# Kernel optimization log

Measured on AMD Instinct MI355X. Metric: run time of the kernel, lower is better.

## Reference

```python
import jax, jax.numpy as jnp
import numpy as np

B, S, D, NH = 4, 1024, 512, 8
HD = D // NH
KN, KL, NC, V = 16384, 8, 4, 6400
EPS = 1e-5
TEMP = 1.0


def _rms(x, w):
    return x * jax.lax.rsqrt(jnp.mean(x * x, axis=-1, keepdims=True) + EPS) * w


def _rope(x, cos, sin):
    # x: [b,s,h,hd]; cos/sin: [s,hd//2] (rotary pairs, minimind complex style)
    xr, xi = x[..., ::2], x[..., 1::2]
    c = cos[None, :, None, :]
    s = sin[None, :, None, :]
    yr = xr * c - xi * s
    yi = xr * s + xi * c
    return jnp.stack([yr, yi], axis=-1).reshape(x.shape)


def setup_inputs() -> dict:
    key = jax.random.key(0)
    ks = jax.random.split(key, 12)
    sc = lambda n: 1.0 / np.sqrt(n)
    inv = 1.0 / (10000.0 ** (np.arange(0, HD, 2) / HD))
    freqs = np.outer(np.arange(S), inv).astype(np.float32)  # [S, HD//2]
    return {
        "x": jax.random.normal(ks[0], (B, S, D), jnp.float32),
        "pos_cos": jnp.asarray(np.cos(freqs)),
        "pos_sin": jnp.asarray(np.sin(freqs)),
        "memory_bank": jax.random.randint(ks[1], (KN, KL), 0, V),
        "tok_emb": jax.random.normal(ks[2], (V, D), jnp.float32) * 0.02,
        "wq": jax.random.normal(ks[3], (D, D), jnp.float32) * sc(D),
        "wk": jax.random.normal(ks[4], (D, D), jnp.float32) * sc(D),
        "wv": jax.random.normal(ks[5], (D, D), jnp.float32) * sc(D),
        "wo": jax.random.normal(ks[6], (D, D), jnp.float32) * sc(D),
        "attn_norm_w": jnp.ones((D,), jnp.float32),
        "mem_norm_w": jnp.ones((D,), jnp.float32),
        "w_gate": jax.random.normal(ks[7], (D, KN), jnp.float32) * sc(D),
        "wg_fuse": jax.random.normal(ks[8], (2 * D, D), jnp.float32) * sc(2 * D),
        "bg_fuse": jnp.zeros((D,), jnp.float32),
        "wm_fuse": jax.random.normal(ks[9], (2 * D, D), jnp.float32) * sc(2 * D),
        "bm_fuse": jnp.zeros((D,), jnp.float32),
        "gumbel_u": jax.random.uniform(ks[10], (B, S, NC), jnp.float32),
    }


def reference(x, pos_cos, pos_sin, memory_bank, tok_emb, wq, wk, wv, wo,
              attn_norm_w, mem_norm_w, w_gate, wg_fuse, bg_fuse, wm_fuse,
              bm_fuse, gumbel_u):
    # --- self attention on attention_norm(x) ---
    hn = _rms(x, attn_norm_w)
    q = _rope((hn @ wq).reshape(B, S, NH, HD), pos_cos, pos_sin)
    k = _rope((hn @ wk).reshape(B, S, NH, HD), pos_cos, pos_sin)
    v = (hn @ wv).reshape(B, S, NH, HD)
    att = jnp.einsum('bqhd,bkhd->bhqk', q, k) * (1.0 / np.sqrt(HD))
    causal = jnp.tril(jnp.ones((S, S), bool))
    att = jnp.where(causal, att, jnp.float32(-1e9))
    p = jax.nn.softmax(att, axis=-1)
    h_attn = jnp.einsum('bhqk,bkhd->bqhd', p, v).reshape(B, S, D) @ wo
    h = x + h_attn

    # --- memory gate: route each token to NC candidate memories ---
    hm = _rms(h_attn, mem_norm_w)                      # memory_norm(h_attn)
    logits = hm @ w_gate                               # [B,S,KN]
    _scores, cand_idx = jax.lax.top_k(logits, NC)      # [B,S,NC]

    # gather memory token ids, embed, mean-pool over knowledge_length
    tok_ids = memory_bank[cand_idx]                    # [B,S,NC,KL]
    cand_mem = tok_emb[tok_ids].mean(axis=3)           # [B,S,NC,D]

    # cosine similarity (torch eps=1e-8 clamp on norms)
    hn2 = jnp.maximum(jnp.linalg.norm(hm, axis=-1), 1e-8)          # [B,S]
    cn2 = jnp.maximum(jnp.linalg.norm(cand_mem, axis=-1), 1e-8)    # [B,S,NC]
    sim = jnp.einsum('bsd,bsnd->bsn', hm, cand_mem) / (hn2[:, :, None] * cn2)

    # gumbel-softmax hard selection with straight-through estimator
    g = -jnp.log(-jnp.log(gumbel_u + 1e-20) + 1e-20)
    soft = jax.nn.softmax((sim + g) / TEMP, axis=-1)
    hard = jax.nn.one_hot(jnp.argmax(soft, axis=-1), NC, dtype=soft.dtype)
    sel_w = hard - jax.lax.stop_gradient(soft) + soft

    similarity_loss = -(sim * sel_w).sum(-1).mean()

    # diversity loss: mean off-diagonal cosine similarity among candidates
    nm = cand_mem / jnp.maximum(jnp.linalg.norm(cand_mem, axis=-1, keepdims=True), 1e-12)
    smat = jnp.einsum('bsnd,bsmd->bsnm', nm, nm)
    eye = jnp.eye(NC, dtype=bool)
    diversity_loss = jnp.where(eye, 0.0, smat).sum() / (B * S * NC * (NC - 1))

    # weighted combine + gated fusion
    sel_mem = jnp.einsum('bsn,bsnd->bsd', sel_w, cand_mem)
    cat = jnp.concatenate([hm, sel_mem], axis=-1)      # [B,S,2D]
    gate = jax.nn.sigmoid(cat @ wg_fuse + bg_fuse)
    memory_output = gate * (cat @ wm_fuse + bm_fuse)
    out = h + memory_output
    return out, similarity_loss, diversity_loss
```

## Files before the change

kernel.cpp:

```cpp
#include <hip/hip_runtime.h>
#include <hip/hip_bf16.h>
#include <math.h>

#define Bn 4
#define Sn 1024
#define Dn 512
#define NHn 8
#define HDn 64
#define KNn 16384
#define KLn 8
#define NCn 4
#define Mn (Bn*Sn)

typedef __attribute__((ext_vector_type(8))) short short8;
typedef __attribute__((ext_vector_type(4))) float f32x4;
typedef unsigned long long u64;

#define MFMA16(a,b,c) __builtin_amdgcn_mfma_f32_16x16x32_bf16(a,b,c,0,0,0)


__device__ __forceinline__ float wred_sum(float v){
  #pragma unroll
  for (int m=1;m<64;m<<=1) v += __shfl_xor(v, m, 64);
  return v;
}

__device__ __forceinline__ ushort f2bf(float f){
  __hip_bfloat16 h = __float2bfloat16(f);
  return __builtin_bit_cast(ushort, h);
}
__device__ __forceinline__ float bf2f(ushort u){
  return __builtin_bit_cast(float, ((unsigned)u)<<16);
}

__device__ __forceinline__ unsigned int fkey(float v){
  unsigned int b = __builtin_bit_cast(unsigned int, v);
  return (b & 0x80000000u) ? ~b : (b | 0x80000000u);
}
__device__ __forceinline__ u64 mkkey(float v, int col){
  return ((u64)fkey(v) << 32) | (u64)(0xFFFFu - (unsigned)col);
}

__device__ __forceinline__ void cex64(u64& a, u64& b){
  u64 mx = a > b ? a : b;
  u64 mn = a > b ? b : a;
  a = mx; b = mn;
}
__device__ __forceinline__ void ins4_64(u64 k, u64&k0,u64&k1,u64&k2,u64&k3){
  if (k > k3){
    k3 = k;
    cex64(k2,k3); cex64(k1,k2); cex64(k0,k1);
  }
}
__device__ __forceinline__ void merge4_64(u64&a0,u64&a1,u64&a2,u64&a3,
                                          u64 b0,u64 b1,u64 b2,u64 b3){
  cex64(a0,b3); cex64(a1,b2); cex64(a2,b1); cex64(a3,b0);
  cex64(a0,a2); cex64(a1,a3);
  cex64(a0,a1); cex64(a2,a3);
}


__global__ __launch_bounds__(256) void rmsnorm_kernel(const float* __restrict__ x,
                                                      const float* __restrict__ w,
                                                      ushort* __restrict__ y){
  int row = blockIdx.x, tid = threadIdx.x;
  const float2* xr = (const float2*)(x + (size_t)row*Dn);
  float2 v = xr[tid];
  float ss = v.x*v.x + v.y*v.y;
  ss = wred_sum(ss);
  __shared__ float red[4];
  int wid = tid>>6, lane = tid&63;
  if (lane==0) red[wid]=ss;
  __syncthreads();
  float tot = red[0]+red[1]+red[2]+red[3];
  float sc = rsqrtf(tot*(1.0f/Dn) + 1e-5f);
  float2 wv = ((const float2*)w)[tid];
  ushort2 u; u.x = f2bf(v.x*sc*wv.x); u.y = f2bf(v.y*sc*wv.y);
  *(ushort2*)&y[(size_t)row*Dn + tid*2] = u;
}


__global__ __launch_bounds__(256) void convT_kernel(const float* __restrict__ src,
                                                    ushort* __restrict__ dst,
                                                    int ldsrc, int lddst){
  __shared__ float T[64][68];
  int tid=threadIdx.x;
  int n0 = blockIdx.x*64, k0 = blockIdx.y*64;
  #pragma unroll
  for (int h=0;h<4;h++){
    int idx = tid + h*256;
    int r = idx>>4, c = (idx&15)*4;
    float4 v = *(const float4*)&src[(size_t)(k0+r)*ldsrc + n0+c];
    *(float4*)&T[r][c] = v;
  }
  __syncthreads();
  #pragma unroll
  for (int h=0;h<4;h++){
    int idx = tid + h*256;
    int n = idx>>4, kc = (idx&15)*4;
    ushort4 u;
    u.x = f2bf(T[kc+0][n]);
    u.y = f2bf(T[kc+1][n]);
    u.z = f2bf(T[kc+2][n]);
    u.w = f2bf(T[kc+3][n]);
    *(ushort4*)&dst[(size_t)(n0+n)*lddst + k0+kc] = u;
  }
}


template<int MODE>
__global__ __launch_bounds__(256) void gemm_bf16(const ushort* __restrict__ A, int lda,
                                                 const ushort* __restrict__ BT, int K,
                                                 void* __restrict__ Cv, int ldc,
                                                 const float* __restrict__ pc,
                                                 const float* __restrict__ ps){
  __shared__ __align__(16) ushort As[64*72];
  __shared__ __align__(16) ushort Bs[64*72];
  int tid=threadIdx.x;
  int w = tid>>6, l = tid&63;
  int wr = w>>1, wc = w&1;
  int g = l>>4, li = l&15;
  int m0 = blockIdx.y*64, n0 = blockIdx.x*64;
  f32x4 acc[2][2] = {};
  for (int kt=0; kt<K; kt+=64){
    #pragma unroll
    for (int t=0;t<2;t++){
      int ch = tid + t*256;
      int r = ch>>3, c = (ch&7)*8;
      *(uint4*)&As[r*72+c] = *(const uint4*)&A [(size_t)(m0+r)*lda + kt + c];
      *(uint4*)&Bs[r*72+c] = *(const uint4*)&BT[(size_t)(n0+r)*K   + kt + c];
    }
    __syncthreads();
    #pragma unroll
    for (int kk=0;kk<2;kk++){
      short8 a0 = *(const short8*)&As[(wr*32 +      li)*72 + kk*32 + g*8];
      short8 a1 = *(const short8*)&As[(wr*32 + 16 + li)*72 + kk*32 + g*8];
      short8 b0 = *(const short8*)&Bs[(wc*32 +      li)*72 + kk*32 + g*8];
      short8 b1 = *(const short8*)&Bs[(wc*32 + 16 + li)*72 + kk*32 + g*8];
      acc[0][0] = MFMA16(a0, b0, acc[0][0]);
      acc[0][1] = MFMA16(a0, b1, acc[0][1]);
      acc[1][0] = MFMA16(a1, b0, acc[1][0]);
      acc[1][1] = MFMA16(a1, b1, acc[1][1]);
    }
    __syncthreads();
  }
  #pragma unroll
  for (int mi=0;mi<2;mi++){
    #pragma unroll
    for (int ni=0;ni<2;ni++){
      #pragma unroll
      for (int reg=0;reg<4;reg++){
        int mm = m0 + wr*32 + mi*16 + g*4 + reg;
        int n  = n0 + wc*32 + ni*16 + li;
        float val = acc[mi][ni][reg];
        if (MODE==0){
          ((float*)Cv)[(size_t)mm*ldc + n] = val;
        } else if (MODE==3){
          ((ushort*)Cv)[(size_t)mm*ldc + n] = f2bf(val);
        } else {
          int b = mm>>10, s2 = mm&1023, h = n>>6, d = n&63;
          size_t o = ((size_t)(b*NHn + h)*Sn + s2)*HDn + d;
          if (MODE==2){
            ((ushort*)Cv)[o] = f2bf(val);
          } else {
            float other = __shfl_xor(val, 1, 64);
            float cc = pc[s2*32 + (d>>1)], snv = ps[s2*32 + (d>>1)];
            float rv = ((li&1)==0) ? val*cc - other*snv : other*snv + val*cc;
            ((ushort*)Cv)[o] = f2bf(rv);
          }
        }
      }
    }
  }
}


__global__ __launch_bounds__(256) void attn_mfma(const ushort* __restrict__ q,
                                                 const ushort* __restrict__ k,
                                                 const ushort* __restrict__ v,
                                                 ushort* __restrict__ o){
  __shared__ __align__(16) ushort Ks[64*72];
  __shared__ __align__(16) ushort VTs[64*64];
  __shared__ __align__(16) ushort Ps[4][16*72];
  int tid = threadIdx.x;
  int w = tid>>6, l = tid&63;
  int g = l>>4, li = l&15;
  int qt = blockIdx.x, bh = blockIdx.y;
  const ushort* Qg = q + ((size_t)bh*Sn + qt*64 + w*16)*HDn;
  const ushort* Kg = k + (size_t)bh*Sn*HDn;
  const ushort* Vg = v + (size_t)bh*Sn*HDn;
  short8 aq0 = *(const short8*)&Qg[(size_t)li*HDn + g*8];
  short8 aq1 = *(const short8*)&Qg[(size_t)li*HDn + 32 + g*8];
  f32x4 oacc[4] = {};
  float mreg[4] = {-1e30f,-1e30f,-1e30f,-1e30f};
  float lreg[4] = {0.f,0.f,0.f,0.f};
  for (int kt=0; kt<=qt; kt++){
    #pragma unroll
    for (int t=0;t<2;t++){
      int ch = tid + t*256;
      int r = ch>>3, c = (ch&7)*8;
      short8 kv8 = *(const short8*)&Kg[(size_t)(kt*64+r)*HDn + c];
      short8 vv8 = *(const short8*)&Vg[(size_t)(kt*64+r)*HDn + c];
      *(short8*)&Ks[r*72 + c] = kv8;
      #pragma unroll
      for (int j=0;j<8;j++){
        int d = c+j;
        int byteoff = d*128 + ((((r>>3) ^ (d>>3)) & 7)<<4) + (r&7)*2;
        *(ushort*)((char*)VTs + byteoff) = (ushort)vv8[j];
      }
    }
    __syncthreads();
    f32x4 s[4] = {};
    #pragma unroll
    for (int n=0;n<4;n++){
      short8 b0 = *(const short8*)&Ks[(n*16+li)*72 + g*8];
      short8 b1 = *(const short8*)&Ks[(n*16+li)*72 + 32 + g*8];
      s[n] = MFMA16(aq0, b0, s[n]);
      s[n] = MFMA16(aq1, b1, s[n]);
    }
    if (kt == qt){
      #pragma unroll
      for (int n=0;n<4;n++){
        int kvg = n*16 + li;
        #pragma unroll
        for (int reg=0;reg<4;reg++){
          int qg = w*16 + g*4 + reg;
          s[n][reg] = (kvg <= qg) ? s[n][reg]*0.125f : -1e9f;
        }
      }
    } else {
      #pragma unroll
      for (int n=0;n<4;n++)
        #pragma unroll
        for (int reg=0;reg<4;reg++) s[n][reg] *= 0.125f;
    }
    #pragma unroll
    for (int reg=0;reg<4;reg++){
      float mt = fmaxf(fmaxf(s[0][reg],s[1][reg]), fmaxf(s[2][reg],s[3][reg]));
      mt = fmaxf(mt, __shfl_xor(mt,1,64));
      mt = fmaxf(mt, __shfl_xor(mt,2,64));
      mt = fmaxf(mt, __shfl_xor(mt,4,64));
      mt = fmaxf(mt, __shfl_xor(mt,8,64));
      float mn = fmaxf(mreg[reg], mt);
      float sc = __expf(mreg[reg]-mn);
      mreg[reg] = mn;
      float p0 = __expf(s[0][reg]-mn), p1 = __expf(s[1][reg]-mn);
      float p2 = __expf(s[2][reg]-mn), p3 = __expf(s[3][reg]-mn);
      s[0][reg]=p0; s[1][reg]=p1; s[2][reg]=p2; s[3][reg]=p3;
      float sm = p0+p1+p2+p3;
      sm += __shfl_xor(sm,1,64);
      sm += __shfl_xor(sm,2,64);
      sm += __shfl_xor(sm,4,64);
      sm += __shfl_xor(sm,8,64);
      lreg[reg] = lreg[reg]*sc + sm;
      #pragma unroll
      for (int n=0;n<4;n++) oacc[n][reg] *= sc;
    }
    #pragma unroll
    for (int n=0;n<4;n++)
      #pragma unroll
      for (int reg=0;reg<4;reg++)
        Ps[w][(g*4+reg)*72 + n*16 + li] = f2bf(s[n][reg]);
    #pragma unroll
    for (int kk=0;kk<2;kk++){
      short8 ap = *(const short8*)&Ps[w][li*72 + kk*32 + g*8];
      #pragma unroll
      for (int n=0;n<4;n++){
        int d = n*16 + li;
        int gran = ((kk*4 + g) ^ (d>>3)) & 7;
        short8 bv = *(const short8*)((char*)VTs + d*128 + (gran<<4));
        oacc[n] = MFMA16(ap, bv, oacc[n]);
      }
    }
    __syncthreads();
  }
  int b = bh>>3, h = bh&7;
  #pragma unroll
  for (int reg=0;reg<4;reg++){
    int qg = qt*64 + w*16 + g*4 + reg;
    float inv = 1.f/lreg[reg];
    #pragma unroll
    for (int n=0;n<4;n++)
      o[((size_t)(b*Sn+qg))*Dn + h*HDn + n*16 + li] = f2bf(oacc[n][reg]*inv);
  }
}


__global__ __launch_bounds__(256) void h_hm_kernel(const float* __restrict__ x,
                                                   const ushort* __restrict__ ha,
                                                   const float* __restrict__ w,
                                                   float* __restrict__ h,
                                                   float* __restrict__ hm32,
                                                   ushort* __restrict__ cat_bf){
  int row=blockIdx.x, tid=threadIdx.x;
  ushort2 a2 = *(const ushort2*)&ha[(size_t)row*Dn + tid*2];
  float ax = bf2f(a2.x), ay = bf2f(a2.y);
  float2 xv = ((const float2*)(x + (size_t)row*Dn))[tid];
  float ss = ax*ax + ay*ay;
  ss = wred_sum(ss);
  __shared__ float red[4];
  int wid=tid>>6, lane=tid&63;
  if (lane==0) red[wid]=ss;
  __syncthreads();
  float tot = red[0]+red[1]+red[2]+red[3];
  float sc = rsqrtf(tot*(1.0f/Dn) + 1e-5f);
  float2 wv = ((const float2*)w)[tid];
  float hm0 = ax*sc*wv.x, hm1 = ay*sc*wv.y;
  ((float2*)(h + (size_t)row*Dn))[tid] = make_float2(xv.x+ax, xv.y+ay);
  ((float2*)(hm32 + (size_t)row*Dn))[tid] = make_float2(hm0, hm1);
  ushort2 u; u.x = f2bf(hm0); u.y = f2bf(hm1);
  *(ushort2*)&cat_bf[(size_t)row*1024 + tid*2] = u;
}


__global__ __launch_bounds__(256) void logits_topk_mfma(const ushort* __restrict__ Abf,
                                                        const ushort* __restrict__ BT,
                                                        u64* __restrict__ keys){
  __shared__ __align__(16) char smem[2*128*40*2];
  ushort* As = (ushort*)smem;
  ushort* Bs = (ushort*)(smem + 128*40*2);
  float*  Ls = (float*)smem;
  int tid=threadIdx.x;
  int w = tid>>6, l = tid&63;
  int wr = w>>1, wc = w&1;
  int g = l>>4, li = l&15;
  int m0 = blockIdx.y*128, n0 = blockIdx.x*128;
  f32x4 acc[4][4] = {};
  for (int kt=0; kt<Dn; kt+=32){
    #pragma unroll
    for (int t=0;t<2;t++){
      int ch = tid + t*256;
      int r = ch>>2, c = (ch&3)*8;
      *(uint4*)&As[r*40+c] = *(const uint4*)&Abf[(size_t)(m0+r)*1024 + kt + c];
      *(uint4*)&Bs[r*40+c] = *(const uint4*)&BT [(size_t)(n0+r)*Dn   + kt + c];
    }
    __syncthreads();
    short8 a[4], b[4];
    #pragma unroll
    for (int i=0;i<4;i++) a[i] = *(const short8*)&As[(wr*64 + i*16 + li)*40 + g*8];
    #pragma unroll
    for (int n=0;n<4;n++) b[n] = *(const short8*)&Bs[(wc*64 + n*16 + li)*40 + g*8];
    #pragma unroll
    for (int i=0;i<4;i++)
      #pragma unroll
      for (int n=0;n<4;n++)
        acc[i][n] = MFMA16(a[i], b[n], acc[i][n]);
    __syncthreads();
  }
  for (int i=0;i<4;i++){
    #pragma unroll
    for (int n=0;n<4;n++)
      #pragma unroll
      for (int reg=0;reg<4;reg++)
        Ls[(wr*16 + g*4 + reg)*132 + wc*64 + n*16 + li] = acc[i][n][reg];
    __syncthreads();
    {
      int r = tid>>3, s = tid&7;
      u64 k0=0,k1=0,k2=0,k3=0;
      #pragma unroll
      for (int c4=0;c4<4;c4++){
        float4 vv = *(const float4*)&Ls[r*132 + s*16 + c4*4];
        int cb = n0 + s*16 + c4*4;
        ins4_64(mkkey(vv.x, cb+0), k0,k1,k2,k3);
        ins4_64(mkkey(vv.y, cb+1), k0,k1,k2,k3);
        ins4_64(mkkey(vv.z, cb+2), k0,k1,k2,k3);
        ins4_64(mkkey(vv.w, cb+3), k0,k1,k2,k3);
      }
      #pragma unroll
      for (int mask=1; mask<8; mask<<=1){
        u64 b0=__shfl_xor(k0,mask,64), b1=__shfl_xor(k1,mask,64);
        u64 b2=__shfl_xor(k2,mask,64), b3=__shfl_xor(k3,mask,64);
        merge4_64(k0,k1,k2,k3, b0,b1,b2,b3);
      }
      if (s==0){
        size_t grow = m0 + ((r>>4)*64 + i*16 + (r&15));
        size_t ob = (grow*128 + blockIdx.x)*4;
        keys[ob+0]=k0; keys[ob+1]=k1; keys[ob+2]=k2; keys[ob+3]=k3;
      }
    }
    __syncthreads();
  }
}


__global__ __launch_bounds__(256) void merge_topk_kernel(const u64* __restrict__ keys,
                                                         int* __restrict__ cand){
  int tid=threadIdx.x, wid=tid>>6, lane=tid&63;
  int row = blockIdx.x*4 + wid;
  size_t base = (size_t)row*512 + (size_t)lane*8;
  u64 k0=keys[base+0],k1=keys[base+1],k2=keys[base+2],k3=keys[base+3];
  merge4_64(k0,k1,k2,k3, keys[base+4],keys[base+5],keys[base+6],keys[base+7]);
  #pragma unroll
  for (int mask=1; mask<64; mask<<=1){
    u64 b0=__shfl_xor(k0,mask,64), b1=__shfl_xor(k1,mask,64);
    u64 b2=__shfl_xor(k2,mask,64), b3=__shfl_xor(k3,mask,64);
    merge4_64(k0,k1,k2,k3, b0,b1,b2,b3);
  }
  if (lane==0){
    cand[(size_t)row*4+0]=(int)(0xFFFFu - (unsigned)(k0 & 0xFFFFu));
    cand[(size_t)row*4+1]=(int)(0xFFFFu - (unsigned)(k1 & 0xFFFFu));
    cand[(size_t)row*4+2]=(int)(0xFFFFu - (unsigned)(k2 & 0xFFFFu));
    cand[(size_t)row*4+3]=(int)(0xFFFFu - (unsigned)(k3 & 0xFFFFu));
  }
}


__global__ __launch_bounds__(256) void select_kernel(const float* __restrict__ hm32,
                                                     const int* __restrict__ cand,
                                                     const int* __restrict__ mem_bank,
                                                     const float* __restrict__ tok_emb,
                                                     const float* __restrict__ gu,
                                                     ushort* __restrict__ cat_bf,
                                                     float* __restrict__ losses){
  __shared__ float cm[4][512];
  __shared__ int ids[32];
  __shared__ float wred[15][4];
  __shared__ int sel_s;
  int row=blockIdx.x, tid=threadIdx.x;
  if (tid<32) ids[tid] = mem_bank[(size_t)cand[(size_t)row*4 + (tid>>3)]*KLn + (tid&7)];
  __syncthreads();
  #pragma unroll
  for (int n=0;n<4;n++){
    float s0=0.f, s1=0.f;
    #pragma unroll
    for (int l=0;l<8;l++){
      const float* e = tok_emb + (size_t)ids[n*8+l]*Dn;
      s0 += e[tid]; s1 += e[tid+256];
    }
    cm[n][tid]=s0*0.125f; cm[n][tid+256]=s1*0.125f;
  }
  __syncthreads();
  float hm0 = hm32[(size_t)row*Dn + tid], hm1 = hm32[(size_t)row*Dn + 256 + tid];
  float c0[4], c1[4];
  #pragma unroll
  for (int n=0;n<4;n++){ c0[n]=cm[n][tid]; c1[n]=cm[n][tid+256]; }
  float p[15];
  p[0]=hm0*hm0+hm1*hm1;
  #pragma unroll
  for (int n=0;n<4;n++) p[1+n]=hm0*c0[n]+hm1*c1[n];
  int qi=5;
  #pragma unroll
  for (int n=0;n<4;n++)
    #pragma unroll
    for (int m=n;m<4;m++) p[qi++]=c0[n]*c0[m]+c1[n]*c1[m];
  int wid=tid>>6, lane=tid&63;
  #pragma unroll
  for (int i=0;i<15;i++) p[i]=wred_sum(p[i]);
  if (lane==0){
    #pragma unroll
    for (int i=0;i<15;i++) wred[i][wid]=p[i];
  }
  __syncthreads();
  if (tid==0){
    float tot[15];
    #pragma unroll
    for (int i=0;i<15;i++) tot[i]=wred[i][0]+wred[i][1]+wred[i][2]+wred[i][3];
    float hn2 = fmaxf(sqrtf(tot[0]), 1e-8f);
    const int diag[4]={5,9,12,14};
    float sim[4], dn[4];
    #pragma unroll
    for (int n=0;n<4;n++){
      float cn = sqrtf(tot[diag[n]]);
      sim[n] = tot[1+n]/(hn2*fmaxf(cn,1e-8f));
      dn[n]  = fmaxf(cn,1e-12f);
    }
    float best=-1e30f; int sel=0;
    #pragma unroll
    for (int n=0;n<4;n++){
      float u = gu[(size_t)row*4+n];
      float g = -logf(-logf(u + 1e-20f) + 1e-20f);
      float a = sim[n]+g;
      if (a>best){ best=a; sel=n; }
    }
    atomicAdd(&losses[0], sim[sel]);
    const int cross[6]={6,7,8,10,11,13};
    const int cn_[6]={0,0,0,1,1,2}, cm_[6]={1,2,3,2,3,3};
    float dv=0.f;
    #pragma unroll
    for (int t=0;t<6;t++) dv += 2.f*tot[cross[t]]/(dn[cn_[t]]*dn[cm_[t]]);
    atomicAdd(&losses[1], dv);
    sel_s=sel;
  }
  __syncthreads();
  int sel=sel_s;
  cat_bf[(size_t)row*1024 + 512 + tid]       = f2bf(cm[sel][tid]);
  cat_bf[(size_t)row*1024 + 512 + 256 + tid] = f2bf(cm[sel][tid+256]);
}


__global__ __launch_bounds__(256) void final_kernel(const float* __restrict__ h,
                                                    const float* __restrict__ g,
                                                    const float* __restrict__ m,
                                                    const float* __restrict__ bg,
                                                    const float* __restrict__ bm,
                                                    const float* __restrict__ losses,
                                                    float* __restrict__ out){
  int idx = blockIdx.x*256 + threadIdx.x;
  int n = idx & (Dn-1);
  float gl = g[idx] + bg[n];
  float ml = m[idx] + bm[n];
  float gate = 1.f/(1.f+__expf(-gl));
  out[idx] = h[idx] + gate*ml;
  if (idx==0){
    out[(size_t)Mn*Dn]     = -losses[0]*(1.f/(float)Mn);
    out[(size_t)Mn*Dn + 1] =  losses[1]*(1.f/(float)(Mn*NCn*(NCn-1)));
  }
}


extern "C" void kernel_launch(void* const* d_in, const int* in_sizes, int n_in,
                              void* d_out, int out_size, void* d_ws, size_t ws_size,
                              hipStream_t stream){
  const float* x           = (const float*)d_in[0];
  const float* pos_cos     = (const float*)d_in[1];
  const float* pos_sin     = (const float*)d_in[2];
  const int*   memory_bank = (const int*)  d_in[3];
  const float* tok_emb     = (const float*)d_in[4];
  const float* wq          = (const float*)d_in[5];
  const float* wk          = (const float*)d_in[6];
  const float* wv          = (const float*)d_in[7];
  const float* wo          = (const float*)d_in[8];
  const float* attn_norm_w = (const float*)d_in[9];
  const float* mem_norm_w  = (const float*)d_in[10];
  const float* w_gate      = (const float*)d_in[11];
  const float* wg_fuse     = (const float*)d_in[12];
  const float* bg_fuse     = (const float*)d_in[13];
  const float* wm_fuse     = (const float*)d_in[14];
  const float* bm_fuse     = (const float*)d_in[15];
  const float* gumbel_u    = (const float*)d_in[16];
  float* out = (float*)d_out;

  char* ws = (char*)d_ws;
  const size_t MB = 1u<<20;
  ushort* BTg       = (ushort*)(ws);
  ushort* wqT       = (ushort*)(ws + 16*MB);
  ushort* wkT       = (ushort*)(ws + 16*MB + 512*1024);
  ushort* wvT       = (ushort*)(ws + 17*MB);
  ushort* woT       = (ushort*)(ws + 17*MB + 512*1024);
  ushort* wgfT      = (ushort*)(ws + 18*MB);
  ushort* wmfT      = (ushort*)(ws + 19*MB);
  ushort* hn_bf     = (ushort*)(ws + 20*MB);
  ushort* pv_bf     = (ushort*)(ws + 20*MB);
  ushort* qb_bf     = (ushort*)(ws + 24*MB);
  ushort* kb_bf     = (ushort*)(ws + 28*MB);
  ushort* vb_bf     = (ushort*)(ws + 32*MB);
  ushort* h_attn_bf = (ushort*)(ws + 36*MB);
  float*  hbuf      = (float*)(ws + 40*MB);
  float*  hm32      = (float*)(ws + 48*MB);
  ushort* cat_bf    = (ushort*)(ws + 56*MB);
  u64*    keys      = (u64*)  (ws + 20*MB);
  float*  gbuf      = (float*)(ws + 20*MB);
  float*  mbuf      = (float*)(ws + 28*MB);
  int*    cand      = (int*)  (ws + 64*MB);
  float*  losses    = (float*)(ws + 64*MB + 65536);

  hipMemsetAsync(losses, 0, 2*sizeof(float), stream);

  convT_kernel<<<dim3(8,8),   256, 0, stream>>>(wq,      wqT,  512,  512);
  convT_kernel<<<dim3(8,8),   256, 0, stream>>>(wk,      wkT,  512,  512);
  convT_kernel<<<dim3(8,8),   256, 0, stream>>>(wv,      wvT,  512,  512);
  convT_kernel<<<dim3(8,8),   256, 0, stream>>>(wo,      woT,  512,  512);
  convT_kernel<<<dim3(8,16),  256, 0, stream>>>(wg_fuse, wgfT, 512,  1024);
  convT_kernel<<<dim3(8,16),  256, 0, stream>>>(wm_fuse, wmfT, 512,  1024);
  convT_kernel<<<dim3(256,8), 256, 0, stream>>>(w_gate,  BTg,  KNn,  512);

  rmsnorm_kernel<<<Mn, 256, 0, stream>>>(x, attn_norm_w, hn_bf);

  dim3 g64(Dn/64, Mn/64);
  gemm_bf16<1><<<g64, 256, 0, stream>>>(hn_bf, 512, wqT, 512, qb_bf, 0, pos_cos, pos_sin);
  gemm_bf16<1><<<g64, 256, 0, stream>>>(hn_bf, 512, wkT, 512, kb_bf, 0, pos_cos, pos_sin);
  gemm_bf16<2><<<g64, 256, 0, stream>>>(hn_bf, 512, wvT, 512, vb_bf, 0, nullptr, nullptr);

  attn_mfma<<<dim3(Sn/64, Bn*NHn), 256, 0, stream>>>(qb_bf, kb_bf, vb_bf, pv_bf);

  gemm_bf16<3><<<g64, 256, 0, stream>>>(pv_bf, 512, woT, 512, h_attn_bf, 512, nullptr, nullptr);

  h_hm_kernel<<<Mn, 256, 0, stream>>>(x, h_attn_bf, mem_norm_w, hbuf, hm32, cat_bf);

  logits_topk_mfma<<<dim3(KNn/128, Mn/128), 256, 0, stream>>>(cat_bf, BTg, keys);
  merge_topk_kernel<<<Mn/4, 256, 0, stream>>>(keys, cand);

  select_kernel<<<Mn, 256, 0, stream>>>(hm32, cand, memory_bank, tok_emb, gumbel_u, cat_bf, losses);

  gemm_bf16<0><<<g64, 256, 0, stream>>>(cat_bf, 1024, wgfT, 1024, gbuf, 512, nullptr, nullptr);
  gemm_bf16<0><<<g64, 256, 0, stream>>>(cat_bf, 1024, wmfT, 1024, mbuf, 512, nullptr, nullptr);

  final_kernel<<<(Mn*Dn)/256, 256, 0, stream>>>(hbuf, gbuf, mbuf, bg_fuse, bm_fuse, losses, out);
}
```

Measured before the change: 563.7 us.

## Replace in-GEMM top-k with group-max, group top-4, and exact recompute; fuse QKV and fuse GEMMs

```diff
diff --git a/kernel.cpp b/kernel.cpp
--- a/kernel.cpp
+++ b/kernel.cpp
@@ -37,8 +37,8 @@
   unsigned int b = __builtin_bit_cast(unsigned int, v);
   return (b & 0x80000000u) ? ~b : (b | 0x80000000u);
 }
-__device__ __forceinline__ u64 mkkey(float v, int col){
-  return ((u64)fkey(v) << 32) | (u64)(0xFFFFu - (unsigned)col);
+__device__ __forceinline__ u64 mkkey(float v, int idx){
+  return ((u64)fkey(v) << 32) | (u64)(0xFFFFu - (unsigned)idx);
 }
 
 __device__ __forceinline__ void cex64(u64& a, u64& b){
@@ -80,12 +80,11 @@
 }
 
 
-__global__ __launch_bounds__(256) void convT_kernel(const float* __restrict__ src,
-                                                    ushort* __restrict__ dst,
-                                                    int ldsrc, int lddst){
+__device__ __forceinline__ void convT_body(const float* __restrict__ src,
+                                           ushort* __restrict__ dst,
+                                           int ldsrc, int lddst,
+                                           int n0, int k0, int tid){
   __shared__ float T[64][68];
-  int tid=threadIdx.x;
-  int n0 = blockIdx.x*64, k0 = blockIdx.y*64;
   #pragma unroll
   for (int h=0;h<4;h++){
     int idx = tid + h*256;
@@ -105,6 +104,30 @@
     u.w = f2bf(T[kc+3][n]);
     *(ushort4*)&dst[(size_t)(n0+n)*lddst + k0+kc] = u;
   }
+}
+
+__global__ __launch_bounds__(256) void convT_kernel(const float* __restrict__ src,
+                                                    ushort* __restrict__ dst,
+                                                    int ldsrc, int lddst){
+  convT_body(src, dst, ldsrc, lddst, blockIdx.x*64, blockIdx.y*64, threadIdx.x);
+}
+
+__global__ __launch_bounds__(256) void convT4_kernel(const float* __restrict__ s0,
+                                                     const float* __restrict__ s1,
+                                                     const float* __restrict__ s2,
+                                                     const float* __restrict__ s3,
+                                                     ushort* __restrict__ dst){
+  const float* src = (blockIdx.z==0)?s0 : (blockIdx.z==1)?s1 : (blockIdx.z==2)?s2 : s3;
+  convT_body(src, dst + (size_t)blockIdx.z*(512*512), 512, 512,
+             blockIdx.x*64, blockIdx.y*64, threadIdx.x);
+}
+
+__global__ __launch_bounds__(256) void convT2_kernel(const float* __restrict__ s0,
+                                                     const float* __restrict__ s1,
+                                                     ushort* __restrict__ dst){
+  const float* src = (blockIdx.z==0)?s0 : s1;
+  convT_body(src, dst + (size_t)blockIdx.z*(512*1024), 512, 1024,
+             blockIdx.x*64, blockIdx.y*64, threadIdx.x);
 }
 
 
@@ -158,9 +181,11 @@
         } else if (MODE==3){
           ((ushort*)Cv)[(size_t)mm*ldc + n] = f2bf(val);
         } else {
-          int b = mm>>10, s2 = mm&1023, h = n>>6, d = n&63;
-          size_t o = ((size_t)(b*NHn + h)*Sn + s2)*HDn + d;
-          if (MODE==2){
+          int which = n>>9, nn = n&511;
+          int b = mm>>10, s2 = mm&1023, h = nn>>6, d = nn&63;
+          size_t o = (size_t)which*((size_t)Mn*Dn)
+                   + ((size_t)(b*NHn + h)*Sn + s2)*HDn + d;
+          if (which==2){
             ((ushort*)Cv)[o] = f2bf(val);
           } else {
             float other = __shfl_xor(val, 1, 64);
@@ -313,13 +338,11 @@
 }
 
 
-__global__ __launch_bounds__(256) void logits_topk_mfma(const ushort* __restrict__ Abf,
-                                                        const ushort* __restrict__ BT,
-                                                        u64* __restrict__ keys){
-  __shared__ __align__(16) char smem[2*128*40*2];
-  ushort* As = (ushort*)smem;
-  ushort* Bs = (ushort*)(smem + 128*40*2);
-  float*  Ls = (float*)smem;
+__global__ __launch_bounds__(256) void logits_gmax(const ushort* __restrict__ Abf,
+                                                   const ushort* __restrict__ BT,
+                                                   float* __restrict__ gmaxT){
+  __shared__ __align__(16) ushort As[128*40];
+  __shared__ __align__(16) ushort Bs[128*40];
   int tid=threadIdx.x;
   int w = tid>>6, l = tid&63;
   int wr = w>>1, wc = w&1;
@@ -344,63 +367,95 @@
     for (int i=0;i<4;i++)
       #pragma unroll
       for (int n=0;n<4;n++)
-        acc[i][n] = MFMA16(a[i], b[n], acc[i][n]);
+        acc[i][n] = MFMA16(b[n], a[i], acc[i][n]);
     __syncthreads();
   }
+  #pragma unroll
   for (int i=0;i<4;i++){
     #pragma unroll
-    for (int n=0;n<4;n++)
-      #pragma unroll
-      for (int reg=0;reg<4;reg++)
-        Ls[(wr*16 + g*4 + reg)*132 + wc*64 + n*16 + li] = acc[i][n][reg];
-    __syncthreads();
-    {
-      int r = tid>>3, s = tid&7;
-      u64 k0=0,k1=0,k2=0,k3=0;
-      #pragma unroll
-      for (int c4=0;c4<4;c4++){
-        float4 vv = *(const float4*)&Ls[r*132 + s*16 + c4*4];
-        int cb = n0 + s*16 + c4*4;
-        ins4_64(mkkey(vv.x, cb+0), k0,k1,k2,k3);
-        ins4_64(mkkey(vv.y, cb+1), k0,k1,k2,k3);
-        ins4_64(mkkey(vv.z, cb+2), k0,k1,k2,k3);
-        ins4_64(mkkey(vv.w, cb+3), k0,k1,k2,k3);
-      }
-      #pragma unroll
-      for (int mask=1; mask<8; mask<<=1){
-        u64 b0=__shfl_xor(k0,mask,64), b1=__shfl_xor(k1,mask,64);
-        u64 b2=__shfl_xor(k2,mask,64), b3=__shfl_xor(k3,mask,64);
-        merge4_64(k0,k1,k2,k3, b0,b1,b2,b3);
-      }
-      if (s==0){
-        size_t grow = m0 + ((r>>4)*64 + i*16 + (r&15));
-        size_t ob = (grow*128 + blockIdx.x)*4;
-        keys[ob+0]=k0; keys[ob+1]=k1; keys[ob+2]=k2; keys[ob+3]=k3;
-      }
-    }
-    __syncthreads();
-  }
-}
-
-
-__global__ __launch_bounds__(256) void merge_topk_kernel(const u64* __restrict__ keys,
-                                                         int* __restrict__ cand){
-  int tid=threadIdx.x, wid=tid>>6, lane=tid&63;
+    for (int n=0;n<4;n++){
+      f32x4 v = acc[i][n];
+      float m = fmaxf(fmaxf(v[0],v[1]), fmaxf(v[2],v[3]));
+      m = fmaxf(m, __shfl_xor(m,16,64));
+      m = fmaxf(m, __shfl_xor(m,32,64));
+      if (g==0)
+        gmaxT[(size_t)(blockIdx.x*8 + wc*4 + n)*Mn + (m0 + wr*64 + i*16 + li)] = m;
+    }
+  }
+}
+
+
+__global__ __launch_bounds__(256) void gmerge_kernel(const float* __restrict__ gmaxT,
+                                                     int* __restrict__ gidx){
+  __shared__ u64 part[64][4][4];
+  int tid=threadIdx.x;
+  int rl = tid&63, ch = tid>>6;
+  int row = blockIdx.x*64 + rl;
+  u64 k0=0,k1=0,k2=0,k3=0;
+  for (int s=0;s<256;s++){
+    int gid = ch*256 + s;
+    float v = gmaxT[(size_t)gid*Mn + row];
+    ins4_64(mkkey(v, gid), k0,k1,k2,k3);
+  }
+  part[rl][ch][0]=k0; part[rl][ch][1]=k1; part[rl][ch][2]=k2; part[rl][ch][3]=k3;
+  __syncthreads();
+  if (tid<64){
+    u64 a0=part[tid][0][0],a1=part[tid][0][1],a2=part[tid][0][2],a3=part[tid][0][3];
+    merge4_64(a0,a1,a2,a3, part[tid][1][0],part[tid][1][1],part[tid][1][2],part[tid][1][3]);
+    merge4_64(a0,a1,a2,a3, part[tid][2][0],part[tid][2][1],part[tid][2][2],part[tid][2][3]);
+    merge4_64(a0,a1,a2,a3, part[tid][3][0],part[tid][3][1],part[tid][3][2],part[tid][3][3]);
+    int r2 = blockIdx.x*64 + tid;
+    gidx[(size_t)r2*4+0] = (int)(0xFFFFu - (unsigned)(a0 & 0xFFFFu));
+    gidx[(size_t)r2*4+1] = (int)(0xFFFFu - (unsigned)(a1 & 0xFFFFu));
+    gidx[(size_t)r2*4+2] = (int)(0xFFFFu - (unsigned)(a2 & 0xFFFFu));
+    gidx[(size_t)r2*4+3] = (int)(0xFFFFu - (unsigned)(a3 & 0xFFFFu));
+  }
+}
+
+
+__global__ __launch_bounds__(256) void recompute_kernel(const ushort* __restrict__ cat_bf,
+                                                        const ushort* __restrict__ BT,
+                                                        const int* __restrict__ gidx,
+                                                        int* __restrict__ cand){
+  __shared__ float hmf[4][512];
+  int tid=threadIdx.x, wid=tid>>6, l=tid&63;
   int row = blockIdx.x*4 + wid;
-  size_t base = (size_t)row*512 + (size_t)lane*8;
-  u64 k0=keys[base+0],k1=keys[base+1],k2=keys[base+2],k3=keys[base+3];
-  merge4_64(k0,k1,k2,k3, keys[base+4],keys[base+5],keys[base+6],keys[base+7]);
+  {
+    uint4 raw = *(const uint4*)&cat_bf[(size_t)row*1024 + l*8];
+    const ushort* u = (const ushort*)&raw;
+    float4 f0 = make_float4(bf2f(u[0]),bf2f(u[1]),bf2f(u[2]),bf2f(u[3]));
+    float4 f1 = make_float4(bf2f(u[4]),bf2f(u[5]),bf2f(u[6]),bf2f(u[7]));
+    *(float4*)&hmf[wid][l*8]   = f0;
+    *(float4*)&hmf[wid][l*8+4] = f1;
+  }
+  __syncthreads();
+  int gid = gidx[(size_t)row*4 + (l>>4)];
+  int col = gid*16 + (l&15);
+  const ushort* bp = BT + (size_t)col*Dn;
+  float a0=0.f,a1=0.f,a2=0.f,a3=0.f;
+  #pragma unroll 8
+  for (int j=0;j<64;j++){
+    short8 bb = *(const short8*)&bp[j*8];
+    float4 h0 = *(const float4*)&hmf[wid][j*8];
+    float4 h1 = *(const float4*)&hmf[wid][j*8+4];
+    a0 += h0.x*bf2f((ushort)bb[0]) + h1.x*bf2f((ushort)bb[4]);
+    a1 += h0.y*bf2f((ushort)bb[1]) + h1.y*bf2f((ushort)bb[5]);
+    a2 += h0.z*bf2f((ushort)bb[2]) + h1.z*bf2f((ushort)bb[6]);
+    a3 += h0.w*bf2f((ushort)bb[3]) + h1.w*bf2f((ushort)bb[7]);
+  }
+  float val = (a0+a1)+(a2+a3);
+  u64 k0 = mkkey(val, col), k1=0, k2=0, k3=0;
   #pragma unroll
   for (int mask=1; mask<64; mask<<=1){
     u64 b0=__shfl_xor(k0,mask,64), b1=__shfl_xor(k1,mask,64);
     u64 b2=__shfl_xor(k2,mask,64), b3=__shfl_xor(k3,mask,64);
     merge4_64(k0,k1,k2,k3, b0,b1,b2,b3);
   }
-  if (lane==0){
-    cand[(size_t)row*4+0]=(int)(0xFFFFu - (unsigned)(k0 & 0xFFFFu));
-    cand[(size_t)row*4+1]=(int)(0xFFFFu - (unsigned)(k1 & 0xFFFFu));
-    cand[(size_t)row*4+2]=(int)(0xFFFFu - (unsigned)(k2 & 0xFFFFu));
-    cand[(size_t)row*4+3]=(int)(0xFFFFu - (unsigned)(k3 & 0xFFFFu));
+  if (l==0){
+    cand[(size_t)row*4+0] = (int)(0xFFFFu - (unsigned)(k0 & 0xFFFFu));
+    cand[(size_t)row*4+1] = (int)(0xFFFFu - (unsigned)(k1 & 0xFFFFu));
+    cand[(size_t)row*4+2] = (int)(0xFFFFu - (unsigned)(k2 & 0xFFFFu));
+    cand[(size_t)row*4+3] = (int)(0xFFFFu - (unsigned)(k3 & 0xFFFFu));
   }
 }
 
@@ -489,16 +544,15 @@
 
 
 __global__ __launch_bounds__(256) void final_kernel(const float* __restrict__ h,
-                                                    const float* __restrict__ g,
-                                                    const float* __restrict__ m,
+                                                    const float* __restrict__ gm,
                                                     const float* __restrict__ bg,
                                                     const float* __restrict__ bm,
                                                     const float* __restrict__ losses,
                                                     float* __restrict__ out){
   int idx = blockIdx.x*256 + threadIdx.x;
-  int n = idx & (Dn-1);
-  float gl = g[idx] + bg[n];
-  float ml = m[idx] + bm[n];
+  int row = idx >> 9, n = idx & (Dn-1);
+  float gl = gm[(size_t)row*1024 + n]       + bg[n];
+  float ml = gm[(size_t)row*1024 + 512 + n] + bm[n];
   float gate = 1.f/(1.f+__expf(-gl));
   out[idx] = h[idx] + gate*ml;
   if (idx==0){
@@ -533,57 +587,51 @@
   char* ws = (char*)d_ws;
   const size_t MB = 1u<<20;
   ushort* BTg       = (ushort*)(ws);
-  ushort* wqT       = (ushort*)(ws + 16*MB);
-  ushort* wkT       = (ushort*)(ws + 16*MB + 512*1024);
-  ushort* wvT       = (ushort*)(ws + 17*MB);
-  ushort* woT       = (ushort*)(ws + 17*MB + 512*1024);
-  ushort* wgfT      = (ushort*)(ws + 18*MB);
-  ushort* wmfT      = (ushort*)(ws + 19*MB);
+  ushort* wqkvT     = (ushort*)(ws + 16*MB);
+  ushort* woT       = wqkvT + 3*(512*512);
+  ushort* wgmT      = (ushort*)(ws + 18*MB);
   ushort* hn_bf     = (ushort*)(ws + 20*MB);
   ushort* pv_bf     = (ushort*)(ws + 20*MB);
-  ushort* qb_bf     = (ushort*)(ws + 24*MB);
-  ushort* kb_bf     = (ushort*)(ws + 28*MB);
-  ushort* vb_bf     = (ushort*)(ws + 32*MB);
+  ushort* qkv_bf    = (ushort*)(ws + 24*MB);
   ushort* h_attn_bf = (ushort*)(ws + 36*MB);
   float*  hbuf      = (float*)(ws + 40*MB);
   float*  hm32      = (float*)(ws + 48*MB);
   ushort* cat_bf    = (ushort*)(ws + 56*MB);
-  u64*    keys      = (u64*)  (ws + 20*MB);
-  float*  gbuf      = (float*)(ws + 20*MB);
-  float*  mbuf      = (float*)(ws + 28*MB);
-  int*    cand      = (int*)  (ws + 64*MB);
-  float*  losses    = (float*)(ws + 64*MB + 65536);
+  float*  gmaxT     = (float*)(ws + 20*MB);
+  float*  gm        = (float*)(ws + 20*MB);
+  int*    gidx      = (int*)  (ws + 36*MB);
+  int*    cand      = (int*)  (ws + 36*MB + 65536);
+  float*  losses    = (float*)(ws + 36*MB + 131072);
 
   hipMemsetAsync(losses, 0, 2*sizeof(float), stream);
 
-  convT_kernel<<<dim3(8,8),   256, 0, stream>>>(wq,      wqT,  512,  512);
-  convT_kernel<<<dim3(8,8),   256, 0, stream>>>(wk,      wkT,  512,  512);
-  convT_kernel<<<dim3(8,8),   256, 0, stream>>>(wv,      wvT,  512,  512);
-  convT_kernel<<<dim3(8,8),   256, 0, stream>>>(wo,      woT,  512,  512);
-  convT_kernel<<<dim3(8,16),  256, 0, stream>>>(wg_fuse, wgfT, 512,  1024);
-  convT_kernel<<<dim3(8,16),  256, 0, stream>>>(wm_fuse, wmfT, 512,  1024);
-  convT_kernel<<<dim3(256,8), 256, 0, stream>>>(w_gate,  BTg,  KNn,  512);
+  convT4_kernel<<<dim3(8,8,4),   256, 0, stream>>>(wq, wk, wv, wo, wqkvT);
+  convT2_kernel<<<dim3(8,16,2),  256, 0, stream>>>(wg_fuse, wm_fuse, wgmT);
+  convT_kernel <<<dim3(256,8),   256, 0, stream>>>(w_gate, BTg, KNn, 512);
 
   rmsnorm_kernel<<<Mn, 256, 0, stream>>>(x, attn_norm_w, hn_bf);
 
-  dim3 g64(Dn/64, Mn/64);
-  gemm_bf16<1><<<g64, 256, 0, stream>>>(hn_bf, 512, wqT, 512, qb_bf, 0, pos_cos, pos_sin);
-  gemm_bf16<1><<<g64, 256, 0, stream>>>(hn_bf, 512, wkT, 512, kb_bf, 0, pos_cos, pos_sin);
-  gemm_bf16<2><<<g64, 256, 0, stream>>>(hn_bf, 512, wvT, 512, vb_bf, 0, nullptr, nullptr);
-
+  gemm_bf16<4><<<dim3(24, Mn/64), 256, 0, stream>>>(hn_bf, 512, wqkvT, 512,
+                                                    qkv_bf, 0, pos_cos, pos_sin);
+
+  ushort* qb_bf = qkv_bf;
+  ushort* kb_bf = qkv_bf + (size_t)Mn*Dn;
+  ushort* vb_bf = qkv_bf + 2*(size_t)Mn*Dn;
   attn_mfma<<<dim3(Sn/64, Bn*NHn), 256, 0, stream>>>(qb_bf, kb_bf, vb_bf, pv_bf);
 
-  gemm_bf16<3><<<g64, 256, 0, stream>>>(pv_bf, 512, woT, 512, h_attn_bf, 512, nullptr, nullptr);
+  gemm_bf16<3><<<dim3(8, Mn/64), 256, 0, stream>>>(pv_bf, 512, woT, 512,
+                                                   h_attn_bf, 512, nullptr, nullptr);
 
   h_hm_kernel<<<Mn, 256, 0, stream>>>(x, h_attn_bf, mem_norm_w, hbuf, hm32, cat_bf);
 
-  logits_topk_mfma<<<dim3(KNn/128, Mn/128), 256, 0, stream>>>(cat_bf, BTg, keys);
-  merge_topk_kernel<<<Mn/4, 256, 0, stream>>>(keys, cand);
+  logits_gmax<<<dim3(KNn/128, Mn/128), 256, 0, stream>>>(cat_bf, BTg, gmaxT);
+  gmerge_kernel<<<Mn/64, 256, 0, stream>>>(gmaxT, gidx);
+  recompute_kernel<<<Mn/4, 256, 0, stream>>>(cat_bf, BTg, gidx, cand);
 
   select_kernel<<<Mn, 256, 0, stream>>>(hm32, cand, memory_bank, tok_emb, gumbel_u, cat_bf, losses);
 
-  gemm_bf16<0><<<g64, 256, 0, stream>>>(cat_bf, 1024, wgfT, 1024, gbuf, 512, nullptr, nullptr);
-  gemm_bf16<0><<<g64, 256, 0, stream>>>(cat_bf, 1024, wmfT, 1024, mbuf, 512, nullptr, nullptr);
-
-  final_kernel<<<(Mn*Dn)/256, 256, 0, stream>>>(hbuf, gbuf, mbuf, bg_fuse, bm_fuse, losses, out);
-}
+  gemm_bf16<0><<<dim3(16, Mn/64), 256, 0, stream>>>(cat_bf, 1024, wgmT, 1024,
+                                                    gm, 1024, nullptr, nullptr);
+
+  final_kernel<<<(Mn*Dn)/256, 256, 0, stream>>>(hbuf, gm, bg_fuse, bm_fuse, losses, out);
+}
```

Result: slower. 581.4 us (+3.1%).
